# Performance work log

Measured on AMD Instinct MI355X. Metric: run time of the kernel, lower is better.

Reference implementation:

```python
import jax, jax.numpy as jnp
import numpy as np


def setup_inputs() -> dict:
    key = jax.random.key(0)
    k1, k2 = jax.random.split(key)
    N, K, D = 262144, 1024, 256
    z_e = jax.random.normal(k1, (N, D), dtype=jnp.float32)
    # torch init: uniform(-1/num_embeddings, 1/num_embeddings)
    codebook = jax.random.uniform(k2, (K, D), dtype=jnp.float32,
                                  minval=-1.0 / K, maxval=1.0 / K)
    return {"z_e": z_e, "codebook": codebook}


def reference(z_e, codebook):
    # distances: ||z||^2 + ||c||^2 - 2 z c^T  -> [N, K]
    distances = (jnp.sum(z_e ** 2, axis=1, keepdims=True)
                 + jnp.sum(codebook ** 2, axis=1)
                 - 2.0 * jnp.matmul(z_e, codebook.T))
    min_encoding_indices = jnp.argmin(distances, axis=1)[:, None]  # [N, 1]
    z_q = codebook[min_encoding_indices[:, 0]]  # [N, D]

    # loss_vq = mse(z_q.detach(), z_e)
    loss_vq = jnp.mean((jax.lax.stop_gradient(z_q) - z_e) ** 2)

    # loss_mean = mse(z_e, mean_codebook.detach())
    mean_codebook = jnp.mean(codebook, axis=0)  # [D]
    loss_mean = jnp.mean((z_e - jax.lax.stop_gradient(mean_codebook)) ** 2)

    # straight-through estimator
    z_q_st = z_e + jax.lax.stop_gradient(z_q - z_e)
    return (z_q_st, loss_vq, loss_mean, min_encoding_indices)
```

## Files before the change

kernel.cpp:

```cpp
#include <hip/hip_runtime.h>


#define NROWS 262144
#define KCODES 1024
#define DDIM 256
#define ND ((size_t)NROWS * (size_t)DDIM)
#define M1F 6e-4f

typedef unsigned int uint;
typedef _Float16 f16x8 __attribute__((ext_vector_type(8)));
typedef float f32x4v __attribute__((ext_vector_type(4)));

__device__ inline float fadd(float a, float b) {
    float d; asm("v_add_f32 %0, %1, %2" : "=v"(d) : "v"(a), "v"(b)); return d;
}
__device__ inline float fmul(float a, float b) {
    float d; asm("v_mul_f32 %0, %1, %2" : "=v"(d) : "v"(a), "v"(b)); return d;
}
__device__ inline float fsub(float a, float b) {
    float d; asm("v_sub_f32 %0, %1, %2" : "=v"(d) : "v"(a), "v"(b)); return d;
}
__device__ inline float ffma(float a, float b, float c) {
    float d; asm("v_fma_f32 %0, %1, %2, %3" : "=v"(d) : "v"(a), "v"(b), "v"(c)); return d;
}

__device__ float np_sq_sum256(const float* __restrict__ a) {
    float tot[2];
    #pragma unroll 1
    for (int h = 0; h < 2; ++h) {
        const float* p = a + h * 128;
        float r[8];
        #pragma unroll
        for (int j = 0; j < 8; ++j) r[j] = fmul(p[j], p[j]);
        #pragma unroll 1
        for (int i = 8; i < 128; i += 8)
            #pragma unroll
            for (int j = 0; j < 8; ++j) r[j] = fadd(r[j], fmul(p[i + j], p[i + j]));
        tot[h] = fadd(fadd(fadd(r[0], r[1]), fadd(r[2], r[3])),
                      fadd(fadd(r[4], r[5]), fadd(r[6], r[7])));
    }
    return fadd(tot[0], tot[1]);
}

__device__ float blas_dot256(const float* __restrict__ zr, const float* __restrict__ cr) {
    float dot = 0.f;
    #pragma unroll 4
    for (int d4 = 0; d4 < 64; ++d4) {
        float4 zz = *(const float4*)(zr + d4 * 4);
        float4 cc = *(const float4*)(cr + d4 * 4);
        dot = ffma(zz.x, cc.x, dot); dot = ffma(zz.y, cc.y, dot);
        dot = ffma(zz.z, cc.z, dot); dot = ffma(zz.w, cc.w, dot);
    }
    return dot;
}

__global__ void k_prep(const float* __restrict__ cb, char* __restrict__ cbh,
                       float* __restrict__ scp, float* __restrict__ mAcc) {
    int bx = blockIdx.x;
    if (bx < 128) {
        int g = bx * 256 + threadIdx.x;
        int t = g >> 10, c = (g >> 5) & 31, j = g & 31;
        const float* s = cb + (size_t)(t * 32 + c) * DDIM + j * 8;
        float4 v0 = *(const float4*)s, v1 = *(const float4*)(s + 4);
        f16x8 h;
        h[0] = (_Float16)(v0.x * 1024.f); h[1] = (_Float16)(v0.y * 1024.f);
        h[2] = (_Float16)(v0.z * 1024.f); h[3] = (_Float16)(v0.w * 1024.f);
        h[4] = (_Float16)(v1.x * 1024.f); h[5] = (_Float16)(v1.y * 1024.f);
        h[6] = (_Float16)(v1.z * 1024.f); h[7] = (_Float16)(v1.w * 1024.f);
        uint byte = (uint)(c * 512 + j * 16) ^ (uint)((c & 7) << 4);
        *(f16x8*)(cbh + (size_t)t * 16384 + byte) = h;
    } else if (bx < 132) {
        int code = (bx - 128) * 256 + threadIdx.x;
        if (code < KCODES) scp[code] = np_sq_sum256(cb + (size_t)code * DDIM);
    } else {
        int d = threadIdx.x;
        int b = bx - 132;
        float s = 0.f;
        for (int i = 0; i < 16; ++i) s += cb[(size_t)(b * 16 + i) * DDIM + d];
        atomicAdd(&mAcc[d], s);
    }
}

__global__ void k_meanfin(const float* __restrict__ mAcc,
                          float* __restrict__ mvec, double* __restrict__ M2p) {
    __shared__ double red[256];
    int d = threadIdx.x;
    float m = mAcc[d] * (1.0f / 1024.0f);
    mvec[d] = m;
    red[d] = (double)m * (double)m;
    __syncthreads();
    for (int off = 128; off; off >>= 1) {
        if (d < off) red[d] += red[d + off];
        __syncthreads();
    }
    if (d == 0) *M2p = red[0];
}

#define GLOAD_LDS16(g, l) \
    __builtin_amdgcn_global_load_lds( \
        (const __attribute__((address_space(1))) void*)(g), \
        (__attribute__((address_space(3))) void*)(l), 16, 0, 0)

__launch_bounds__(256)
__global__ void k_main(const float* __restrict__ z, const char* __restrict__ cbh,
                       const float* __restrict__ sc, const float* __restrict__ mvec,
                       float* __restrict__ out, uint* __restrict__ counts,
                       uint2* __restrict__ listTri, uint* __restrict__ listFull,
                       int capTri, int capFull,
                       double* __restrict__ lossA, double* __restrict__ lossB) {
    __shared__ char tiles[2][16384] __attribute__((aligned(16)));
    __shared__ float sc_lds[1024];
    __shared__ float statA[128], statZM[128];
    __shared__ float lred[2];

    const int tid = threadIdx.x;
    const int wave = tid >> 6;
    const int lane = tid & 63;
    const int l15 = lane & 15;
    const int lg = lane >> 4;
    const int blockRow = blockIdx.x * 128;

    if (tid < 2) lred[tid] = 0.f;
    for (int i = tid; i < 1024; i += 256) sc_lds[i] = sc[i];

    f16x8 za[2][8];
    #pragma unroll
    for (int m = 0; m < 2; ++m) {
        const float* zr = z + (size_t)(blockRow + wave * 32 + m * 16 + l15) * DDIM;
        float a2 = 0.f, zm = 0.f;
        #pragma unroll
        for (int kk = 0; kk < 8; ++kk) {
            int d0 = kk * 32 + lg * 8;
            float4 v0 = *(const float4*)(zr + d0);
            float4 v1 = *(const float4*)(zr + d0 + 4);
            float4 w0 = *(const float4*)(mvec + d0);
            float4 w1 = *(const float4*)(mvec + d0 + 4);
            a2 += v0.x * v0.x + v0.y * v0.y + v0.z * v0.z + v0.w * v0.w;
            a2 += v1.x * v1.x + v1.y * v1.y + v1.z * v1.z + v1.w * v1.w;
            zm += v0.x * w0.x + v0.y * w0.y + v0.z * w0.z + v0.w * w0.w;
            zm += v1.x * w1.x + v1.y * w1.y + v1.z * w1.z + v1.w * w1.w;
            f16x8 h;
            h[0] = (_Float16)v0.x; h[1] = (_Float16)v0.y;
            h[2] = (_Float16)v0.z; h[3] = (_Float16)v0.w;
            h[4] = (_Float16)v1.x; h[5] = (_Float16)v1.y;
            h[6] = (_Float16)v1.z; h[7] = (_Float16)v1.w;
            za[m][kk] = h;
        }
        a2 += __shfl_xor(a2, 16); a2 += __shfl_xor(a2, 32);
        zm += __shfl_xor(zm, 16); zm += __shfl_xor(zm, 32);
        if (lg == 0) {
            statA[wave * 32 + m * 16 + l15] = a2;
            statZM[wave * 32 + m * 16 + l15] = zm;
        }
    }
    __syncthreads();

    float k1v[2][2][4], k2v[2][2][4], k3v[2][2][4];
    #pragma unroll
    for (int n = 0; n < 2; ++n)
        #pragma unroll
        for (int m = 0; m < 2; ++m)
            #pragma unroll
            for (int r = 0; r < 4; ++r) {
                k1v[n][m][r] = 3e38f; k2v[n][m][r] = 3e38f; k3v[n][m][r] = 3e38f;
            }

    const char* gsrc0 = cbh + (size_t)wave * 4096 + (size_t)lane * 16;
    #define STAGE(T, BUF) { \
        const char* g_ = gsrc0 + (size_t)(T) * 16384; \
        char* l_ = &tiles[BUF][wave * 4096]; \
        _Pragma("unroll") \
        for (int i_ = 0; i_ < 4; ++i_) GLOAD_LDS16(g_ + i_ * 1024, l_ + i_ * 1024); \
    }

    #define COMPUTE(T, BUF) { \
        f32x4v acc[2][2]; \
        _Pragma("unroll") \
        for (int m = 0; m < 2; ++m) \
            _Pragma("unroll") \
            for (int n = 0; n < 2; ++n) acc[m][n] = (f32x4v){0.f, 0.f, 0.f, 0.f}; \
        const char* tb = &tiles[BUF][0]; \
        _Pragma("unroll") \
        for (int kk = 0; kk < 8; ++kk) { \
            _Pragma("unroll") \
            for (int n = 0; n < 2; ++n) { \
                int lcode = n * 16 + l15; \
                uint byte = (uint)(lcode * 512 + kk * 64 + lg * 16) ^ (uint)((lcode & 7) << 4); \
                f16x8 b = *(const f16x8*)(tb + byte); \
                acc[0][n] = __builtin_amdgcn_mfma_f32_16x16x32_f16(za[0][kk], b, acc[0][n], 0, 0, 0); \
                acc[1][n] = __builtin_amdgcn_mfma_f32_16x16x32_f16(za[1][kk], b, acc[1][n], 0, 0, 0); \
            } \
        } \
        int tbase = (T) * 32; \
        _Pragma("unroll") \
        for (int n = 0; n < 2; ++n) { \
            int codev = tbase + n * 16 + l15; \
            float scv = sc_lds[codev]; \
            _Pragma("unroll") \
            for (int m = 0; m < 2; ++m) \
                _Pragma("unroll") \
                for (int r = 0; r < 4; ++r) { \
                    float s = fmaf(acc[m][n][r], -0.001953125f, scv); \
                    uint kb = (__float_as_uint(s) & 0xFFFFFC00u) | (uint)codev; \
                    float k = __uint_as_float(kb); \
                    float o1 = k1v[n][m][r], o2 = k2v[n][m][r]; \
                    k3v[n][m][r] = __builtin_amdgcn_fmed3f(o2, k3v[n][m][r], k); \
                    k2v[n][m][r] = __builtin_amdgcn_fmed3f(o1, o2, k); \
                    k1v[n][m][r] = fminf(o1, k); \
                } \
        } \
    }

    STAGE(0, 0);
    #pragma unroll 1
    for (int t = 0; t < 31; ++t) {
        STAGE(t + 1, (t + 1) & 1);
        asm volatile("s_waitcnt vmcnt(4)" ::: "memory");
        __builtin_amdgcn_s_barrier();
        __builtin_amdgcn_sched_barrier(0);
        COMPUTE(t, t & 1);
        __builtin_amdgcn_sched_barrier(0);
        __builtin_amdgcn_s_barrier();
    }
    asm volatile("s_waitcnt vmcnt(0)" ::: "memory");
    __builtin_amdgcn_s_barrier();
    __builtin_amdgcn_sched_barrier(0);
    COMPUTE(31, 1);

    float lA = 0.f, lB = 0.f;
    #pragma unroll
    for (int m = 0; m < 2; ++m)
        #pragma unroll
        for (int r = 0; r < 4; ++r) {
            float x1 = k1v[0][m][r], x2 = k2v[0][m][r], x3 = k3v[0][m][r];
            float y1 = k1v[1][m][r], y2 = k2v[1][m][r], y3 = k3v[1][m][r];
            float mx = fmaxf(x1, y1);
            float a3 = fminf(fminf(__builtin_amdgcn_fmed3f(x2, y2, mx), x3), y3);
            float a2 = fminf(fminf(mx, x2), y2);
            float a1 = fminf(x1, y1);
            #pragma unroll
            for (int mk = 1; mk <= 8; mk <<= 1) {
                float b1 = __shfl_xor(a1, mk);
                float b2 = __shfl_xor(a2, mk);
                float b3 = __shfl_xor(a3, mk);
                float mx2 = fmaxf(a1, b1);
                float n3 = fminf(fminf(__builtin_amdgcn_fmed3f(a2, b2, mx2), a3), b3);
                float n2 = fminf(fminf(mx2, a2), b2);
                a1 = fminf(a1, b1); a2 = n2; a3 = n3;
            }
            if (l15 == 0) {
                int rowL = wave * 32 + m * 16 + lg * 4 + r;
                int row = blockRow + rowL;
                int i1 = (int)(__float_as_uint(a1) & 1023u);
                int i2 = (int)(__float_as_uint(a2) & 1023u);
                int i3 = (int)(__float_as_uint(a3) & 1023u);
                int flag = (a3 - a1 < M1F) ? 2 : ((a2 - a1 < M1F) ? 1 : 0);
                float slotval = (float)i1;
                if (flag == 2) {
                    uint p = atomicAdd(&counts[1], 1u);
                    if (p < (uint)capFull) listFull[p] = (uint)row;
                    else slotval = (float)(i1 | (1 << 20));
                } else if (flag == 1) {
                    uint p = atomicAdd(&counts[0], 1u);
                    if (p < (uint)capTri)
                        listTri[p] = make_uint2((uint)row, (uint)(i1 | (i2 << 10) | (i3 << 20)));
                    else slotval = (float)(i1 | (1 << 20));
                }
                out[ND + 2 + (size_t)row] = slotval;
                lA += statA[rowL] + a1;
                lB += statA[rowL] - 2.f * statZM[rowL];
            }
        }
    if (l15 == 0) { atomicAdd(&lred[0], lA); atomicAdd(&lred[1], lB); }
    __syncthreads();
    if (tid == 0) {
        atomicAdd(lossA, (double)lred[0]);
        atomicAdd(lossB, (double)lred[1]);
    }
}

__launch_bounds__(256)
__global__ void k_refine_tri(const float* __restrict__ z, const float* __restrict__ cb,
                             const float* __restrict__ scp,
                             const uint* __restrict__ counts,
                             const uint2* __restrict__ listTri, int capTri,
                             float* __restrict__ out) {
    __shared__ float B[4][4][256];
    const int wv = threadIdx.x >> 6;
    const int lane = threadIdx.x & 63;
    uint n = counts[0];
    if (n > (uint)capTri) n = (uint)capTri;
    uint nw = gridDim.x * 4;
    for (uint it = blockIdx.x * 4 + wv; it < n; it += nw) {
        uint2 e = listTri[it];
        int row = (int)e.x;
        int i1 = (int)(e.y & 1023), i2 = (int)((e.y >> 10) & 1023), i3 = (int)((e.y >> 20) & 1023);
        *(float4*)&B[wv][0][lane * 4] = *(const float4*)(z + (size_t)row * DDIM + lane * 4);
        *(float4*)&B[wv][1][lane * 4] = *(const float4*)(cb + (size_t)i1 * DDIM + lane * 4);
        *(float4*)&B[wv][2][lane * 4] = *(const float4*)(cb + (size_t)i2 * DDIM + lane * 4);
        *(float4*)&B[wv][3][lane * 4] = *(const float4*)(cb + (size_t)i3 * DDIM + lane * 4);
        asm volatile("s_waitcnt vmcnt(0) lgkmcnt(0)" ::: "memory");
        float A = np_sq_sum256(B[wv][0]);
        float dA = 0.f, dB = 0.f, dC = 0.f;
        #pragma unroll 4
        for (int d4 = 0; d4 < 64; ++d4) {
            float4 zz = *(const float4*)&B[wv][0][d4 * 4];
            float4 ca = *(const float4*)&B[wv][1][d4 * 4];
            float4 cc = *(const float4*)&B[wv][2][d4 * 4];
            float4 cd = *(const float4*)&B[wv][3][d4 * 4];
            dA = ffma(zz.x, ca.x, dA); dA = ffma(zz.y, ca.y, dA);
            dA = ffma(zz.z, ca.z, dA); dA = ffma(zz.w, ca.w, dA);
            dB = ffma(zz.x, cc.x, dB); dB = ffma(zz.y, cc.y, dB);
            dB = ffma(zz.z, cc.z, dB); dB = ffma(zz.w, cc.w, dB);
            dC = ffma(zz.x, cd.x, dC); dC = ffma(zz.y, cd.y, dC);
            dC = ffma(zz.z, cd.z, dC); dC = ffma(zz.w, cd.w, dC);
        }
        float d1 = fsub(fadd(A, scp[i1]), fmul(2.f, dA));
        float d2 = fsub(fadd(A, scp[i2]), fmul(2.f, dB));
        float d3 = fsub(fadd(A, scp[i3]), fmul(2.f, dC));
        int win = i1; float bd = d1;
        if (d2 < bd || (d2 == bd && i2 < win)) { bd = d2; win = i2; }
        if (d3 < bd || (d3 == bd && i3 < win)) { bd = d3; win = i3; }
        if (win != i1 && lane == 0) out[ND + 2 + (size_t)row] = (float)win;
    }
}

__launch_bounds__(256, 2)
__global__ void k_refine_full(const float* __restrict__ z, const float* __restrict__ cb,
                              const float* __restrict__ scp,
                              const uint* __restrict__ counts,
                              const uint* __restrict__ listFull, int capFull,
                              float* __restrict__ out) {
    __shared__ float zrow[256];
    __shared__ float avs[256];
    __shared__ int ais[256];

    uint n = counts[1];
    if (n > (uint)capFull) n = (uint)capFull;
    const int tid = threadIdx.x;

    for (uint j = blockIdx.x; j < n; j += gridDim.x) {
        int row = (int)listFull[j];
        __syncthreads();
        if (tid < 64)
            *(float4*)&zrow[tid * 4] = *(const float4*)(z + (size_t)row * DDIM + tid * 4);
        __syncthreads();

        float A = np_sq_sum256(zrow);

        float d0 = 0.f, d1 = 0.f, d2 = 0.f, d3 = 0.f;
        const float* c0 = cb + (size_t)(tid + 0) * DDIM;
        const float* c1 = cb + (size_t)(tid + 256) * DDIM;
        const float* c2 = cb + (size_t)(tid + 512) * DDIM;
        const float* c3 = cb + (size_t)(tid + 768) * DDIM;
        #pragma unroll 4
        for (int q = 0; q < 64; ++q) {
            float4 zz = *(const float4*)&zrow[q * 4];
            float4 a = *(const float4*)(c0 + q * 4);
            float4 b = *(const float4*)(c1 + q * 4);
            float4 c = *(const float4*)(c2 + q * 4);
            float4 d = *(const float4*)(c3 + q * 4);
            d0 = ffma(zz.x, a.x, d0); d0 = ffma(zz.y, a.y, d0);
            d0 = ffma(zz.z, a.z, d0); d0 = ffma(zz.w, a.w, d0);
            d1 = ffma(zz.x, b.x, d1); d1 = ffma(zz.y, b.y, d1);
            d1 = ffma(zz.z, b.z, d1); d1 = ffma(zz.w, b.w, d1);
            d2 = ffma(zz.x, c.x, d2); d2 = ffma(zz.y, c.y, d2);
            d2 = ffma(zz.z, c.z, d2); d2 = ffma(zz.w, c.w, d2);
            d3 = ffma(zz.x, d.x, d3); d3 = ffma(zz.y, d.y, d3);
            d3 = ffma(zz.z, d.z, d3); d3 = ffma(zz.w, d.w, d3);
        }
        float best = 1e30f; int bi = 0x7fffffff;
        float dd[4] = {d0, d1, d2, d3};
        #pragma unroll
        for (int kk = 0; kk < 4; ++kk) {
            int code = tid + kk * 256;
            float dist = fsub(fadd(A, scp[code]), fmul(2.f, dd[kk]));
            if (dist < best || (dist == best && code < bi)) { best = dist; bi = code; }
        }
        avs[tid] = best; ais[tid] = bi;
        __syncthreads();
        for (int off = 128; off; off >>= 1) {
            if (tid < off) {
                float o = avs[tid + off]; int oi = ais[tid + off];
                if (o < avs[tid] || (o == avs[tid] && oi < ais[tid])) {
                    avs[tid] = o; ais[tid] = oi;
                }
            }
            __syncthreads();
        }
        if (tid == 0) out[ND + 2 + (size_t)row] = (float)ais[0];
    }
}

__global__ void k_sweep(const float* __restrict__ z, const float* __restrict__ cb,
                        const float* __restrict__ scp, float* __restrict__ out) {
    int row = blockIdx.x * 256 + threadIdx.x;
    float v = out[ND + 2 + (size_t)row];
    if (v < 1048576.f) return;
    const float* zr = z + (size_t)row * DDIM;
    float A = np_sq_sum256(zr);
    float best = 1e30f; int win = 0x7fffffff;
    for (int code = 0; code < KCODES; ++code) {
        float dot = blas_dot256(zr, cb + (size_t)code * DDIM);
        float dist = fsub(fadd(A, scp[code]), fmul(2.f, dot));
        if (dist < best) { best = dist; win = code; }
    }
    out[ND + 2 + (size_t)row] = (float)win;
}

__global__ void k_gather(const float* __restrict__ cb, float* __restrict__ out) {
    __shared__ int idx[128];
    const int tid = threadIdx.x;
    const int blockRow = blockIdx.x * 128;
    if (tid < 128) idx[tid] = ((int)out[ND + 2 + (size_t)(blockRow + tid)]) & 1023;
    __syncthreads();
    float4* out4 = (float4*)out;
    const float4* cb4 = (const float4*)cb;
    #pragma unroll 4
    for (int i = 0; i < 32; ++i) {
        int q = i * 256 + tid;
        int rowL = q >> 6, ch = q & 63;
        int code = idx[rowL];
        out4[(size_t)(blockRow + rowL) * 64 + ch] = cb4[(size_t)code * 64 + ch];
    }
}

__global__ void k_final(const double* __restrict__ lossA, const double* __restrict__ lossB,
                        const double* __restrict__ M2p, float* __restrict__ out) {
    if (threadIdx.x == 0) {
        double nd = (double)ND;
        out[ND] = (float)(*lossA / nd);
        out[ND + 1] = (float)((*lossB + (double)NROWS * (*M2p)) / nd);
    }
}

extern "C" void kernel_launch(void* const* d_in, const int* in_sizes, int n_in,
                              void* d_out, int out_size, void* d_ws, size_t ws_size,
                              hipStream_t stream) {
    const float* z = (const float*)d_in[0];
    const float* cb = (const float*)d_in[1];
    float* out = (float*)d_out;

    double* lossA = (double*)d_ws;
    double* lossB = lossA + 1;
    double* M2p   = lossA + 2;
    uint*   counts = (uint*)((char*)d_ws + 24);
    float*  mAcc  = (float*)((char*)d_ws + 32);
    float*  mvec  = (float*)((char*)d_ws + 2048);
    float*  scp   = (float*)((char*)d_ws + 4096);
    char*   cbh   = (char*)d_ws + 8192;

    size_t base = 8192 + 524288;
    size_t avail = ws_size > base ? ws_size - base : 0;
    int capFull = (int)(avail / 24);
    if (capFull > 32768) capFull = 32768;
    size_t fullBytes = ((size_t)capFull * 4 + 7) & ~(size_t)7;
    size_t availTri = avail > fullBytes ? avail - fullBytes : 0;
    int capTri = (int)(availTri / 8);
    if (capTri > 131072) capTri = 131072;

    uint*  listFull = (uint*)((char*)d_ws + base);
    uint2* listTri  = (uint2*)((char*)d_ws + base + fullBytes);

    hipMemsetAsync(d_ws, 0, 1056, stream);
    k_prep<<<196, 256, 0, stream>>>(cb, cbh, scp, mAcc);
    k_meanfin<<<1, 256, 0, stream>>>(mAcc, mvec, M2p);
    k_main<<<NROWS / 128, 256, 0, stream>>>(z, cbh, scp, mvec, out,
                                            counts, listTri, listFull,
                                            capTri, capFull, lossA, lossB);
    k_refine_tri<<<2048, 256, 0, stream>>>(z, cb, scp, counts, listTri, capTri, out);
    k_refine_full<<<2048, 256, 0, stream>>>(z, cb, scp, counts, listFull, capFull, out);
    k_sweep<<<NROWS / 256, 256, 0, stream>>>(z, cb, scp, out);
    k_gather<<<NROWS / 128, 256, 0, stream>>>(cb, out);
    k_final<<<1, 64, 0, stream>>>(lossA, lossB, M2p, out);
}
```

Baseline: 929.2 us.

## Fuse refine, sweep and gather into a per-block tail kernel

Replaces the global atomic work lists and the separate refine-tri, refine-full, sweep and gather kernels with one k_tail kernel. k_main now encodes ambiguity flags and candidate indices into the index slot. k_tail rebuilds the ambiguous rows per 128-row block in LDS, refines pair candidates and full-scan rows locally, then gathers codebook rows. This removes global atomics, several launches and the grid-wide sweep. The trade-off is that refinement is no longer load-balanced across the GPU, so blocks with many ambiguous rows may lag, and the third candidate is dropped from the pair refinement.

New measurement: 834.3 us. 10.2% less time.

```diff
diff --git a/kernel.cpp b/kernel.cpp
--- a/kernel.cpp
+++ b/kernel.cpp
@@ -40,18 +40,6 @@
                       fadd(fadd(r[4], r[5]), fadd(r[6], r[7])));
     }
     return fadd(tot[0], tot[1]);
-}
-
-__device__ float blas_dot256(const float* __restrict__ zr, const float* __restrict__ cr) {
-    float dot = 0.f;
-    #pragma unroll 4
-    for (int d4 = 0; d4 < 64; ++d4) {
-        float4 zz = *(const float4*)(zr + d4 * 4);
-        float4 cc = *(const float4*)(cr + d4 * 4);
-        dot = ffma(zz.x, cc.x, dot); dot = ffma(zz.y, cc.y, dot);
-        dot = ffma(zz.z, cc.z, dot); dot = ffma(zz.w, cc.w, dot);
-    }
-    return dot;
 }
 
 __global__ void k_prep(const float* __restrict__ cb, char* __restrict__ cbh,
@@ -104,9 +92,7 @@
 __launch_bounds__(256)
 __global__ void k_main(const float* __restrict__ z, const char* __restrict__ cbh,
                        const float* __restrict__ sc, const float* __restrict__ mvec,
-                       float* __restrict__ out, uint* __restrict__ counts,
-                       uint2* __restrict__ listTri, uint* __restrict__ listFull,
-                       int capTri, int capFull,
+                       float* __restrict__ out,
                        double* __restrict__ lossA, double* __restrict__ lossB) {
     __shared__ char tiles[2][16384] __attribute__((aligned(16)));
     __shared__ float sc_lds[1024];
@@ -253,20 +239,11 @@
                 int row = blockRow + rowL;
                 int i1 = (int)(__float_as_uint(a1) & 1023u);
                 int i2 = (int)(__float_as_uint(a2) & 1023u);
-                int i3 = (int)(__float_as_uint(a3) & 1023u);
                 int flag = (a3 - a1 < M1F) ? 2 : ((a2 - a1 < M1F) ? 1 : 0);
-                float slotval = (float)i1;
-                if (flag == 2) {
-                    uint p = atomicAdd(&counts[1], 1u);
-                    if (p < (uint)capFull) listFull[p] = (uint)row;
-                    else slotval = (float)(i1 | (1 << 20));
-                } else if (flag == 1) {
-                    uint p = atomicAdd(&counts[0], 1u);
-                    if (p < (uint)capTri)
-                        listTri[p] = make_uint2((uint)row, (uint)(i1 | (i2 << 10) | (i3 << 20)));
-                    else slotval = (float)(i1 | (1 << 20));
-                }
-                out[ND + 2 + (size_t)row] = slotval;
+                int enc = (flag == 2) ? (i1 | (2 << 20))
+                        : (flag == 1) ? (i1 | (i2 << 10) | (1 << 20))
+                                      : i1;
+                out[ND + 2 + (size_t)row] = (float)enc;
                 lA += statA[rowL] + a1;
                 lB += statA[rowL] - 2.f * statZM[rowL];
             }
@@ -280,74 +257,78 @@
 }
 
 __launch_bounds__(256)
-__global__ void k_refine_tri(const float* __restrict__ z, const float* __restrict__ cb,
-                             const float* __restrict__ scp,
-                             const uint* __restrict__ counts,
-                             const uint2* __restrict__ listTri, int capTri,
-                             float* __restrict__ out) {
-    __shared__ float B[4][4][256];
-    const int wv = threadIdx.x >> 6;
-    const int lane = threadIdx.x & 63;
-    uint n = counts[0];
-    if (n > (uint)capTri) n = (uint)capTri;
-    uint nw = gridDim.x * 4;
-    for (uint it = blockIdx.x * 4 + wv; it < n; it += nw) {
-        uint2 e = listTri[it];
-        int row = (int)e.x;
-        int i1 = (int)(e.y & 1023), i2 = (int)((e.y >> 10) & 1023), i3 = (int)((e.y >> 20) & 1023);
-        *(float4*)&B[wv][0][lane * 4] = *(const float4*)(z + (size_t)row * DDIM + lane * 4);
-        *(float4*)&B[wv][1][lane * 4] = *(const float4*)(cb + (size_t)i1 * DDIM + lane * 4);
-        *(float4*)&B[wv][2][lane * 4] = *(const float4*)(cb + (size_t)i2 * DDIM + lane * 4);
-        *(float4*)&B[wv][3][lane * 4] = *(const float4*)(cb + (size_t)i3 * DDIM + lane * 4);
+__global__ void k_tail(const float* __restrict__ z, const float* __restrict__ cb,
+                       const float* __restrict__ scp, float* __restrict__ out) {
+    __shared__ int idx[128];
+    __shared__ uint pairList[128];
+    __shared__ int fullList[128];
+    __shared__ int cnts[2];
+    __shared__ float PB[4][3][256];
+    __shared__ float zrow[256];
+    __shared__ float avs[256];
+    __shared__ int ais[256];
+
+    const int tid = threadIdx.x;
+    const int wv = tid >> 6;
+    const int lane = tid & 63;
+    const int blockRow = blockIdx.x * 128;
+
+    if (tid < 2) cnts[tid] = 0;
+    __syncthreads();
+    if (tid < 128) {
+        int enc = (int)out[ND + 2 + (size_t)(blockRow + tid)];
+        idx[tid] = enc & 1023;
+        if (enc >= (1 << 20)) {
+            if ((enc >> 20) == 1) {
+                int p = atomicAdd(&cnts[0], 1);
+                pairList[p] = (uint)tid | ((uint)(enc & 0xFFFFF) << 7);
+            } else {
+                int p = atomicAdd(&cnts[1], 1);
+                fullList[p] = tid;
+            }
+        }
+    }
+    __syncthreads();
+    int nPair = cnts[0], nFull = cnts[1];
+
+    for (int e = wv; e < nPair; e += 4) {
+        uint pe = pairList[e];
+        int rowL = (int)(pe & 127u);
+        int i1 = (int)((pe >> 7) & 1023u);
+        int i2 = (int)((pe >> 17) & 1023u);
+        int row = blockRow + rowL;
+        *(float4*)&PB[wv][0][lane * 4] = *(const float4*)(z + (size_t)row * DDIM + lane * 4);
+        *(float4*)&PB[wv][1][lane * 4] = *(const float4*)(cb + (size_t)i1 * DDIM + lane * 4);
+        *(float4*)&PB[wv][2][lane * 4] = *(const float4*)(cb + (size_t)i2 * DDIM + lane * 4);
         asm volatile("s_waitcnt vmcnt(0) lgkmcnt(0)" ::: "memory");
-        float A = np_sq_sum256(B[wv][0]);
-        float dA = 0.f, dB = 0.f, dC = 0.f;
+        float A = np_sq_sum256(PB[wv][0]);
+        float dA = 0.f, dB = 0.f;
         #pragma unroll 4
         for (int d4 = 0; d4 < 64; ++d4) {
-            float4 zz = *(const float4*)&B[wv][0][d4 * 4];
-            float4 ca = *(const float4*)&B[wv][1][d4 * 4];
-            float4 cc = *(const float4*)&B[wv][2][d4 * 4];
-            float4 cd = *(const float4*)&B[wv][3][d4 * 4];
+            float4 zz = *(const float4*)&PB[wv][0][d4 * 4];
+            float4 ca = *(const float4*)&PB[wv][1][d4 * 4];
+            float4 cc = *(const float4*)&PB[wv][2][d4 * 4];
             dA = ffma(zz.x, ca.x, dA); dA = ffma(zz.y, ca.y, dA);
             dA = ffma(zz.z, ca.z, dA); dA = ffma(zz.w, ca.w, dA);
             dB = ffma(zz.x, cc.x, dB); dB = ffma(zz.y, cc.y, dB);
             dB = ffma(zz.z, cc.z, dB); dB = ffma(zz.w, cc.w, dB);
-            dC = ffma(zz.x, cd.x, dC); dC = ffma(zz.y, cd.y, dC);
-            dC = ffma(zz.z, cd.z, dC); dC = ffma(zz.w, cd.w, dC);
         }
         float d1 = fsub(fadd(A, scp[i1]), fmul(2.f, dA));
         float d2 = fsub(fadd(A, scp[i2]), fmul(2.f, dB));
-        float d3 = fsub(fadd(A, scp[i3]), fmul(2.f, dC));
-        int win = i1; float bd = d1;
-        if (d2 < bd || (d2 == bd && i2 < win)) { bd = d2; win = i2; }
-        if (d3 < bd || (d3 == bd && i3 < win)) { bd = d3; win = i3; }
-        if (win != i1 && lane == 0) out[ND + 2 + (size_t)row] = (float)win;
-    }
-}
-
-__launch_bounds__(256, 2)
-__global__ void k_refine_full(const float* __restrict__ z, const float* __restrict__ cb,
-                              const float* __restrict__ scp,
-                              const uint* __restrict__ counts,
-                              const uint* __restrict__ listFull, int capFull,
-                              float* __restrict__ out) {
-    __shared__ float zrow[256];
-    __shared__ float avs[256];
-    __shared__ int ais[256];
-
-    uint n = counts[1];
-    if (n > (uint)capFull) n = (uint)capFull;
-    const int tid = threadIdx.x;
-
-    for (uint j = blockIdx.x; j < n; j += gridDim.x) {
-        int row = (int)listFull[j];
+        int win = (d2 < d1 || (d2 == d1 && i2 < i1)) ? i2 : i1;
+        if (lane == 0) idx[rowL] = win;
+    }
+    __syncthreads();
+
+    #pragma unroll 1
+    for (int e = 0; e < nFull; ++e) {
+        int rowL = fullList[e];
+        int row = blockRow + rowL;
         __syncthreads();
         if (tid < 64)
             *(float4*)&zrow[tid * 4] = *(const float4*)(z + (size_t)row * DDIM + tid * 4);
         __syncthreads();
-
         float A = np_sq_sum256(zrow);
-
         float d0 = 0.f, d1 = 0.f, d2 = 0.f, d3 = 0.f;
         const float* c0 = cb + (size_t)(tid + 0) * DDIM;
         const float* c1 = cb + (size_t)(tid + 256) * DDIM;
@@ -388,32 +369,12 @@
             }
             __syncthreads();
         }
-        if (tid == 0) out[ND + 2 + (size_t)row] = (float)ais[0];
-    }
-}
-
-__global__ void k_sweep(const float* __restrict__ z, const float* __restrict__ cb,
-                        const float* __restrict__ scp, float* __restrict__ out) {
-    int row = blockIdx.x * 256 + threadIdx.x;
-    float v = out[ND + 2 + (size_t)row];
-    if (v < 1048576.f) return;
-    const float* zr = z + (size_t)row * DDIM;
-    float A = np_sq_sum256(zr);
-    float best = 1e30f; int win = 0x7fffffff;
-    for (int code = 0; code < KCODES; ++code) {
-        float dot = blas_dot256(zr, cb + (size_t)code * DDIM);
-        float dist = fsub(fadd(A, scp[code]), fmul(2.f, dot));
-        if (dist < best) { best = dist; win = code; }
-    }
-    out[ND + 2 + (size_t)row] = (float)win;
-}
-
-__global__ void k_gather(const float* __restrict__ cb, float* __restrict__ out) {
-    __shared__ int idx[128];
-    const int tid = threadIdx.x;
-    const int blockRow = blockIdx.x * 128;
-    if (tid < 128) idx[tid] = ((int)out[ND + 2 + (size_t)(blockRow + tid)]) & 1023;
-    __syncthreads();
+        if (tid == 0) idx[rowL] = ais[0];
+        __syncthreads();
+    }
+    __syncthreads();
+
+    if (tid < 128) out[ND + 2 + (size_t)(blockRow + tid)] = (float)idx[tid];
     float4* out4 = (float4*)out;
     const float4* cb4 = (const float4*)cb;
     #pragma unroll 4
@@ -444,33 +405,15 @@
     double* lossA = (double*)d_ws;
     double* lossB = lossA + 1;
     double* M2p   = lossA + 2;
-    uint*   counts = (uint*)((char*)d_ws + 24);
     float*  mAcc  = (float*)((char*)d_ws + 32);
     float*  mvec  = (float*)((char*)d_ws + 2048);
     float*  scp   = (float*)((char*)d_ws + 4096);
     char*   cbh   = (char*)d_ws + 8192;
 
-    size_t base = 8192 + 524288;
-    size_t avail = ws_size > base ? ws_size - base : 0;
-    int capFull = (int)(avail / 24);
-    if (capFull > 32768) capFull = 32768;
-    size_t fullBytes = ((size_t)capFull * 4 + 7) & ~(size_t)7;
-    size_t availTri = avail > fullBytes ? avail - fullBytes : 0;
-    int capTri = (int)(availTri / 8);
-    if (capTri > 131072) capTri = 131072;
-
-    uint*  listFull = (uint*)((char*)d_ws + base);
-    uint2* listTri  = (uint2*)((char*)d_ws + base + fullBytes);
-
     hipMemsetAsync(d_ws, 0, 1056, stream);
     k_prep<<<196, 256, 0, stream>>>(cb, cbh, scp, mAcc);
     k_meanfin<<<1, 256, 0, stream>>>(mAcc, mvec, M2p);
-    k_main<<<NROWS / 128, 256, 0, stream>>>(z, cbh, scp, mvec, out,
-                                            counts, listTri, listFull,
-                                            capTri, capFull, lossA, lossB);
-    k_refine_tri<<<2048, 256, 0, stream>>>(z, cb, scp, counts, listTri, capTri, out);
-    k_refine_full<<<2048, 256, 0, stream>>>(z, cb, scp, counts, listFull, capFull, out);
-    k_sweep<<<NROWS / 256, 256, 0, stream>>>(z, cb, scp, out);
-    k_gather<<<NROWS / 128, 256, 0, stream>>>(cb, out);
+    k_main<<<NROWS / 128, 256, 0, stream>>>(z, cbh, scp, mvec, out, lossA, lossB);
+    k_tail<<<NROWS / 128, 256, 0, stream>>>(z, cb, scp, out);
     k_final<<<1, 64, 0, stream>>>(lossA, lossB, M2p, out);
 }
```
